# Kernel tuning notes

Measured on AMD Instinct MI355X. Metric: run time of the kernel, lower is better.

Reference implementation:

```python
import jax, jax.numpy as jnp
import numpy as np

B, N, D, H, NCB, TOPK = 4, 2048, 256, 2048, 256, 16
DP = D // 4
SCALE = float(np.sqrt(DP))
THRESH = 0.7
EPS = 1e-8


def setup_inputs() -> dict:
    key = jax.random.key(0)
    ks = jax.random.split(key, 12)
    g = lambda i, shape, s=1.0: jax.random.normal(ks[i], shape, jnp.float32) * s
    return {
        "agent_states": g(0, (B, N, D)),
        "agent_actions": g(1, (B, N, D)),
        "episodic_mem": g(2, (B, N, H)),
        "Wq": g(3, (D, DP), 0.05), "bq": jnp.zeros((DP,), jnp.float32),
        "Wk": g(4, (D, DP), 0.05), "bk": jnp.zeros((DP,), jnp.float32),
        "log_temp": jnp.asarray(0.0, jnp.float32),
        "Wc": g(5, (D, DP), 0.05), "bc": jnp.zeros((DP,), jnp.float32),
        "temp_coal": jnp.asarray(10.0, jnp.float32),
        "W_to_hdc": g(6, (D, H), 0.05), "b_to_hdc": jnp.zeros((H,), jnp.float32),
        "W_from_hdc": g(7, (H, D), 0.02), "b_from_hdc": jnp.zeros((D,), jnp.float32),
        "agent_keys": jnp.sign(g(8, (N, H))),
        "position_codes": jnp.sign(g(9, (NCB, H))),
        "step": 3,
    }


def _cosine(a, b):
    # torch F.cosine_similarity semantics, dim=-1, eps=1e-8
    na = jnp.maximum(jnp.linalg.norm(a, axis=-1), EPS)
    nb = jnp.maximum(jnp.linalg.norm(b, axis=-1), EPS)
    return jnp.sum(a * b, axis=-1) / (na * nb)


def _to_hdc_ste(x):
    soft = jnp.tanh(x * 3.0)
    hard = jnp.sign(x)
    hard = jnp.where(hard == 0, jnp.ones_like(hard), hard)
    return soft + jax.lax.stop_gradient(hard - soft)


def reference(agent_states, agent_actions, episodic_mem, Wq, bq, Wk, bk,
              log_temp, Wc, bc, temp_coal, W_to_hdc, b_to_hdc,
              W_from_hdc, b_from_hdc, agent_keys, position_codes, step):
    # ---- DynamicGraph.compute_graph: top-k dynamic attention adjacency ----
    Q = agent_actions @ Wq + bq                      # (B,N,DP)
    K = agent_actions @ Wk + bk                      # (B,N,DP)
    temp = jnp.clip(jnp.exp(log_temp), 0.1, 10.0)
    scores = jnp.einsum('bnd,bmd->bnm', Q, K) / (SCALE * temp)   # (B,N,N)
    _, topk_idx = jax.lax.top_k(scores, TOPK)                     # (B,N,k)
    bI = jnp.arange(B)[:, None, None]
    nI = jnp.arange(N)[None, :, None]
    mask = jnp.zeros_like(scores).at[bI, nI, topk_idx].set(1.0)   # scatter, like torch scatter_
    scores = scores * mask + (1.0 - mask) * -1e9
    adjacency = jax.nn.softmax(scores, axis=-1)
    # message passing over dynamic graph
    incoming = jnp.einsum('bnm,bmd->bnd', adjacency, agent_states)

    # ---- AgentCombination: sigmoid-normalized coalition mixing ----
    proj = agent_actions @ Wc + bc                   # (B,N,DP)
    pn = proj / jnp.maximum(jnp.linalg.norm(proj, axis=-1, keepdims=True), 1e-12)
    sim = jnp.einsum('bnd,bmd->bnm', pn, pn)
    cw = jax.nn.sigmoid((sim - THRESH) * temp_coal)
    cw = cw / (jnp.sum(cw, axis=-1, keepdims=True) + EPS)
    combined = jnp.einsum('bnm,bmd->bnd', cw, incoming)
    mixed = 0.8 * incoming + 0.2 * combined          # (B,N,D)

    # ---- HDCMemory: bind / write / read with STE ----
    q = _to_hdc_ste(mixed @ W_to_hdc + b_to_hdc)     # (B,N,H) bipolar via STE
    pq = q * agent_keys[None]                        # bind with agent key
    mem = jax.lax.stop_gradient(episodic_mem)        # memory read is detached in original
    pos_code = position_codes[step % NCB]            # (H,)
    new_mem = 0.95 * mem + 0.05 * (q * pos_code)     # write: bind + decay bundle
    strength = jax.nn.sigmoid(_cosine(new_mem, pq))[..., None]   # read similarity
    recall = (new_mem @ W_from_hdc + b_from_hdc) * strength      # (B,N,D)
    return mixed + recall
```

## Files before the change

### kernel.cpp

```cpp
#include <hip/hip_runtime.h>
#include <math.h>

#define BATCH 4
#define NN 2048
#define DD 256
#define HH 2048
#define DP 64
#define KTOP 16

typedef float f32x4 __attribute__((ext_vector_type(4)));
typedef short short8 __attribute__((ext_vector_type(8)));
typedef short short4v __attribute__((ext_vector_type(4)));

__device__ __forceinline__ short f2bf(float x) {
    union { float f; unsigned u; } v; v.f = x;
    unsigned r = v.u + 0x7FFFu + ((v.u >> 16) & 1u);
    return (short)(r >> 16);
}
__device__ __forceinline__ float bf2f(short s) {
    union { unsigned u; float f; } v; v.u = ((unsigned)(unsigned short)s) << 16;
    return v.f;
}

__global__ __launch_bounds__(64) void proj_kernel(
    const float* __restrict__ act,
    const float* __restrict__ Wq, const float* __restrict__ bq,
    const float* __restrict__ Wk, const float* __restrict__ bk,
    const float* __restrict__ Wc, const float* __restrict__ bc,
    float* __restrict__ Qo, float* __restrict__ Ko, short* __restrict__ Pno)
{
    const int row0 = blockIdx.x * 4;
    const int t = threadIdx.x;
    __shared__ float rowbuf[4][DD];
    const float* src = act + (size_t)row0 * DD;
    for (int i = t; i < 4 * DD; i += 64) rowbuf[i >> 8][i & 255] = src[i];
    __syncthreads();

    float q[4], k[4], c[4];
    #pragma unroll
    for (int r = 0; r < 4; ++r) { q[r] = bq[t]; k[r] = bk[t]; c[r] = bc[t]; }

    for (int d = 0; d < DD; ++d) {
        float wq = Wq[d * DP + t];
        float wk = Wk[d * DP + t];
        float wc = Wc[d * DP + t];
        #pragma unroll
        for (int r = 0; r < 4; ++r) {
            float av = rowbuf[r][d];
            q[r] = fmaf(av, wq, q[r]);
            k[r] = fmaf(av, wk, k[r]);
            c[r] = fmaf(av, wc, c[r]);
        }
    }
    #pragma unroll
    for (int r = 0; r < 4; ++r) {
        float ss = c[r] * c[r];
        #pragma unroll
        for (int off = 32; off; off >>= 1) ss += __shfl_xor(ss, off);
        float nrm = fmaxf(sqrtf(ss), 1e-12f);
        size_t o = (size_t)(row0 + r) * DP + t;
        Qo[o] = q[r];
        Ko[o] = k[r];
        Pno[o] = f2bf(c[r] / nrm);
    }
}

__global__ __launch_bounds__(256) void prep_kernel(
    const float* __restrict__ W2h, const float* __restrict__ Wfh,
    short* __restrict__ W2hT_hi, short* __restrict__ W2hT_lo,
    short* __restrict__ WfhT_hi, short* __restrict__ WfhT_lo)
{
    int b = blockIdx.x;
    const float* src; short *dhi, *dlo; int R, C, r0, c0;
    if (b < 512) {
        src = W2h; dhi = W2hT_hi; dlo = W2hT_lo; R = 256; C = 2048;
        r0 = (b >> 6) * 32; c0 = (b & 63) * 32;
    } else {
        b -= 512;
        src = Wfh; dhi = WfhT_hi; dlo = WfhT_lo; R = 2048; C = 256;
        r0 = (b >> 3) * 32; c0 = (b & 7) * 32;
    }
    int tx = threadIdx.x & 31, ty = threadIdx.x >> 5;
    __shared__ float tile[32][33];
    #pragma unroll
    for (int i = 0; i < 4; ++i)
        tile[ty + 8 * i][tx] = src[(size_t)(r0 + ty + 8 * i) * C + c0 + tx];
    __syncthreads();
    #pragma unroll
    for (int i = 0; i < 4; ++i) {
        float v = tile[tx][ty + 8 * i];
        short hi = f2bf(v);
        size_t o = (size_t)(c0 + ty + 8 * i) * R + r0 + tx;
        dhi[o] = hi;
        dlo[o] = f2bf(v - bf2f(hi));
    }
}

__global__ __launch_bounds__(512, 4) void attn_score_kernel(
    const float* __restrict__ Q, const float* __restrict__ K,
    const float* __restrict__ log_temp,
    float* __restrict__ selw_g, int* __restrict__ seli_g)
{
    const int t = threadIdx.x;
    const int w = t >> 6, l = t & 63;
    const int row = blockIdx.x * 8 + w;
    const int b = row >> 11;

    __shared__ float Ksh[128][68];

    const float temp = fminf(fmaxf(expf(log_temp[0]), 0.1f), 10.0f);
    const float scale = 1.0f / (8.0f * temp);

    const float* Kb = K + (size_t)b * NN * DP;
    const float4* qr4 = (const float4*)(Q + (size_t)row * DP);

    float sc[32];

    for (int ch = 0; ch < 16; ++ch) {
        __syncthreads();
        {
            int r = t >> 2, seg = t & 3;
            const float4* src = (const float4*)(Kb + (size_t)(ch * 128 + r) * DP + seg * 16);
            float4* dst = (float4*)&Ksh[r][seg * 16];
            dst[0] = src[0]; dst[1] = src[1]; dst[2] = src[2]; dst[3] = src[3];
        }
        __syncthreads();
        float a0 = 0.f, a1 = 0.f;
        const float4* k0 = (const float4*)&Ksh[l][0];
        const float4* k1 = (const float4*)&Ksh[64 + l][0];
        #pragma unroll
        for (int h = 0; h < 2; ++h) {
            float4 q[8];
            #pragma unroll
            for (int i = 0; i < 8; ++i) q[i] = qr4[h * 8 + i];
            #pragma unroll
            for (int i = 0; i < 8; ++i) {
                float4 kv0 = k0[h * 8 + i];
                float4 kv1 = k1[h * 8 + i];
                a0 = fmaf(kv0.x, q[i].x, fmaf(kv0.y, q[i].y, fmaf(kv0.z, q[i].z, fmaf(kv0.w, q[i].w, a0))));
                a1 = fmaf(kv1.x, q[i].x, fmaf(kv1.y, q[i].y, fmaf(kv1.z, q[i].z, fmaf(kv1.w, q[i].w, a1))));
            }
        }
        sc[ch * 2]     = a0 * scale;
        sc[ch * 2 + 1] = a1 * scale;
    }

    float wv = 0.f; int wm = 0;
    for (int it = 0; it < KTOP; ++it) {
        float bv = sc[0]; int bs = 0;
        #pragma unroll
        for (int i = 1; i < 32; ++i) {
            bool g = sc[i] > bv;
            bv = g ? sc[i] : bv;
            bs = g ? i : bs;
        }
        int bm = (bs >> 1) * 128 + (bs & 1) * 64 + l;
        #pragma unroll
        for (int off = 1; off < 64; off <<= 1) {
            float ov = __shfl_xor(bv, off);
            int   om = __shfl_xor(bm, off);
            bool take = (ov > bv) || (ov == bv && om < bm);
            bv = take ? ov : bv;
            bm = take ? om : bm;
        }
        if (l == it) { wv = bv; wm = bm; }
        if ((bm & 63) == l) {
            int s = ((bm >> 7) << 1) | ((bm >> 6) & 1);
            #pragma unroll
            for (int i = 0; i < 32; ++i) if (s == i) sc[i] = -3.0e38f;
        }
    }

    float mx = __shfl(wv, 0);
    float e = (l < KTOP) ? expf(wv - mx) : 0.f;
    float Z = e;
    #pragma unroll
    for (int off = 1; off < 64; off <<= 1) Z += __shfl_xor(Z, off);
    if (l < KTOP) {
        selw_g[(size_t)row * KTOP + l] = e / Z;
        seli_g[(size_t)row * KTOP + l] = wm;
    }
}

__global__ __launch_bounds__(256) void gather_kernel(
    const float* __restrict__ selw_g, const int* __restrict__ seli_g,
    const float* __restrict__ states, float* __restrict__ incoming)
{
    const int t = threadIdx.x;
    const int w = t >> 6, l = t & 63;
    const int row = blockIdx.x * 4 + w;
    const int b = row >> 11;

    float wv = 0.f; int mi = 0;
    if (l < KTOP) {
        wv = selw_g[(size_t)row * KTOP + l];
        mi = seli_g[(size_t)row * KTOP + l];
    }
    const float* Sb = states + (size_t)b * NN * DD;
    f32x4 acc = (f32x4){0.f, 0.f, 0.f, 0.f};
    #pragma unroll
    for (int kk = 0; kk < KTOP; ++kk) {
        float wk = __shfl(wv, kk);
        int   ik = __shfl(mi, kk);
        const float4 v = *(const float4*)(Sb + (size_t)ik * DD + l * 4);
        acc[0] = fmaf(wk, v.x, acc[0]);
        acc[1] = fmaf(wk, v.y, acc[1]);
        acc[2] = fmaf(wk, v.z, acc[2]);
        acc[3] = fmaf(wk, v.w, acc[3]);
    }
    *(float4*)(incoming + (size_t)row * DD + l * 4) = *(float4*)&acc;
}

__global__ __launch_bounds__(256) void coal_kernel(
    const short* __restrict__ pnb_g, const float* __restrict__ incoming,
    const float* __restrict__ temp_coal, float* __restrict__ mixed)
{
    const int b  = blockIdx.x >> 7;
    const int rem = blockIdx.x & 127;
    const int n0 = (rem >> 1) * 32;
    const int dh = rem & 1;
    const int t = threadIdx.x;
    const int w = t >> 6;
    const int l = t & 63;

    __shared__ alignas(16) short pnA[32][72];
    __shared__ alignas(16) short pnB[64][72];
    __shared__ alignas(16) short cwt[32][72];
    __shared__ alignas(16) short incT[128][72];
    __shared__ float rowsum[32];

    const size_t bbase = (size_t)b * NN;

    {
        int r = t >> 3, k8 = (t & 7) * 8;
        *(short8*)&pnA[r][k8] = *(const short8*)(pnb_g + (bbase + n0 + r) * DP + k8);
    }
    if (t < 32) rowsum[t] = 0.0f;

    const float tc = temp_coal[0];

    f32x4 acc[2][2];
    #pragma unroll
    for (int i = 0; i < 2; ++i)
        #pragma unroll
        for (int j = 0; j < 2; ++j)
            acc[i][j] = (f32x4){0.f, 0.f, 0.f, 0.f};

    const int lrow = l & 15;
    const int lk   = (l >> 4) * 8;

    for (int ch = 0; ch < 32; ++ch) {
        const int m0 = ch * 64;
        __syncthreads();

        {
            int r = t >> 2, kq = (t & 3) * 16;
            const short* src = pnb_g + (bbase + m0 + r) * DP + kq;
            *(short8*)&pnB[r][kq]     = *(const short8*)src;
            *(short8*)&pnB[r][kq + 8] = *(const short8*)(src + 8);
        }
        {
            int d4 = t & 31;
            int mg = t >> 5;
            const float* incb = incoming + (bbase + m0) * DD + dh * 128 + d4 * 4;
            #pragma unroll
            for (int i = 0; i < 8; ++i) {
                int m = mg * 8 + i;
                float4 v = *(const float4*)(incb + (size_t)m * DD);
                int db = d4 * 4;
                incT[db + 0][m] = f2bf(v.x);
                incT[db + 1][m] = f2bf(v.y);
                incT[db + 2][m] = f2bf(v.z);
                incT[db + 3][m] = f2bf(v.w);
            }
        }
        __syncthreads();

        f32x4 sacc[2];
        sacc[0] = (f32x4){0.f, 0.f, 0.f, 0.f};
        sacc[1] = (f32x4){0.f, 0.f, 0.f, 0.f};
        #pragma unroll
        for (int ks = 0; ks < 2; ++ks) {
            short8 bfr = *(const short8*)&pnB[w * 16 + lrow][lk + ks * 32];
            short8 a0  = *(const short8*)&pnA[lrow][lk + ks * 32];
            short8 a1  = *(const short8*)&pnA[16 + lrow][lk + ks * 32];
            sacc[0] = __builtin_amdgcn_mfma_f32_16x16x32_bf16(a0, bfr, sacc[0], 0, 0, 0);
            sacc[1] = __builtin_amdgcn_mfma_f32_16x16x32_bf16(a1, bfr, sacc[1], 0, 0, 0);
        }
        #pragma unroll
        for (int rt = 0; rt < 2; ++rt) {
            #pragma unroll
            for (int j = 0; j < 4; ++j) {
                int rr = rt * 16 + (l >> 4) * 4 + j;
                int cc = w * 16 + lrow;
                float cv = 1.0f / (1.0f + expf(-(sacc[rt][j] - 0.7f) * tc));
                cwt[rr][cc] = f2bf(cv);
            }
        }
        __syncthreads();

        {
            int r = t >> 3, c8 = (t & 7) * 8;
            short8 cv = *(const short8*)&cwt[r][c8];
            float p = 0.f;
            #pragma unroll
            for (int j = 0; j < 8; ++j) p += bf2f(cv[j]);
            p += __shfl_xor(p, 1);
            p += __shfl_xor(p, 2);
            p += __shfl_xor(p, 4);
            if ((t & 7) == 0) rowsum[r] += p;
        }

        #pragma unroll
        for (int ks = 0; ks < 2; ++ks) {
            short8 a0 = *(const short8*)&cwt[lrow][lk + ks * 32];
            short8 a1 = *(const short8*)&cwt[16 + lrow][lk + ks * 32];
            #pragma unroll
            for (int ct = 0; ct < 2; ++ct) {
                short8 bfr = *(const short8*)&incT[w * 32 + ct * 16 + lrow][lk + ks * 32];
                acc[0][ct] = __builtin_amdgcn_mfma_f32_16x16x32_bf16(a0, bfr, acc[0][ct], 0, 0, 0);
                acc[1][ct] = __builtin_amdgcn_mfma_f32_16x16x32_bf16(a1, bfr, acc[1][ct], 0, 0, 0);
            }
        }
    }
    __syncthreads();

    #pragma unroll
    for (int rt = 0; rt < 2; ++rt) {
        #pragma unroll
        for (int ct = 0; ct < 2; ++ct) {
            #pragma unroll
            for (int j = 0; j < 4; ++j) {
                int rr = rt * 16 + (l >> 4) * 4 + j;
                int cc = w * 32 + ct * 16 + lrow;
                float inv = 1.0f / (rowsum[rr] + 1e-8f);
                float comb = acc[rt][ct][j] * inv;
                size_t gi = (bbase + n0 + rr) * DD + dh * 128 + cc;
                mixed[gi] = 0.8f * incoming[gi] + 0.2f * comb;
            }
        }
    }
}

__global__ __launch_bounds__(256) void hdcA_kernel(
    const float* __restrict__ mixed,
    const short* __restrict__ W2hT_hi, const short* __restrict__ W2hT_lo,
    const float* __restrict__ b2h,
    unsigned short* __restrict__ qbits)
{
    const int rb = blockIdx.x >> 3;
    const int hs = blockIdx.x & 7;
    const int row0 = rb * 32;
    const int hbase = hs * 256;
    const int t = threadIdx.x;
    const int w = t >> 6, l = t & 63;
    const int lr = l & 15, lg = l >> 4;

    __shared__ short Ahi[32][264], Alo[32][264];
    __shared__ short Whi[64][136], Wlo[64][136];

    #pragma unroll
    for (int i = 0; i < 8; ++i) {
        int idx = t + i * 256;
        int r = idx >> 6, c = (idx & 63) * 4;
        float4 v = *(const float4*)(mixed + (size_t)(row0 + r) * DD + c);
        short4v hi4, lo4;
        hi4[0] = f2bf(v.x); lo4[0] = f2bf(v.x - bf2f(hi4[0]));
        hi4[1] = f2bf(v.y); lo4[1] = f2bf(v.y - bf2f(hi4[1]));
        hi4[2] = f2bf(v.z); lo4[2] = f2bf(v.z - bf2f(hi4[2]));
        hi4[3] = f2bf(v.w); lo4[3] = f2bf(v.w - bf2f(hi4[3]));
        *(short4v*)&Ahi[r][c] = hi4;
        *(short4v*)&Alo[r][c] = lo4;
    }

    for (int ch = 0; ch < 4; ++ch) {
        const int h0 = hbase + ch * 64;
        f32x4 zac[2];
        zac[0] = (f32x4){0.f, 0.f, 0.f, 0.f};
        zac[1] = (f32x4){0.f, 0.f, 0.f, 0.f};
        #pragma unroll
        for (int ks = 0; ks < 2; ++ks) {
            const int k0 = ks * 128;
            __syncthreads();
            {
                int r = t >> 2, cb = (t & 3) * 32;
                const short* sh = W2hT_hi + (size_t)(h0 + r) * DD + k0 + cb;
                const short* sl = W2hT_lo + (size_t)(h0 + r) * DD + k0 + cb;
                #pragma unroll
                for (int j = 0; j < 4; ++j) {
                    *(short8*)&Whi[r][cb + j * 8] = *(const short8*)(sh + j * 8);
                    *(short8*)&Wlo[r][cb + j * 8] = *(const short8*)(sl + j * 8);
                }
            }
            __syncthreads();
            #pragma unroll
            for (int kt = 0; kt < 4; ++kt) {
                int kk = k0 + kt * 32 + lg * 8;
                int kw = kt * 32 + lg * 8;
                short8 bhi = *(const short8*)&Whi[w * 16 + lr][kw];
                short8 blo = *(const short8*)&Wlo[w * 16 + lr][kw];
                #pragma unroll
                for (int mt = 0; mt < 2; ++mt) {
                    short8 ahi = *(const short8*)&Ahi[mt * 16 + lr][kk];
                    short8 alo = *(const short8*)&Alo[mt * 16 + lr][kk];
                    zac[mt] = __builtin_amdgcn_mfma_f32_16x16x32_bf16(ahi, bhi, zac[mt], 0, 0, 0);
                    zac[mt] = __builtin_amdgcn_mfma_f32_16x16x32_bf16(ahi, blo, zac[mt], 0, 0, 0);
                    zac[mt] = __builtin_amdgcn_mfma_f32_16x16x32_bf16(alo, bhi, zac[mt], 0, 0, 0);
                }
            }
        }
        const float bv = b2h[h0 + w * 16 + lr];
        #pragma unroll
        for (int mt = 0; mt < 2; ++mt) {
            #pragma unroll
            for (int j = 0; j < 4; ++j) {
                float z = zac[mt][j] + bv;
                unsigned long long bal = __ballot(z >= 0.0f);
                if (lr == 0)
                    qbits[(size_t)(row0 + mt * 16 + lg * 4 + j) * 128 + (h0 >> 4) + w] =
                        (unsigned short)((bal >> (lg * 16)) & 0xFFFFull);
            }
        }
    }
}

__global__ __launch_bounds__(512) void hdcB_kernel(
    const float* __restrict__ mem, const unsigned short* __restrict__ qbits,
    const float* __restrict__ pos_codes, const int* __restrict__ step,
    const short* __restrict__ WfhT_hi,
    const float* __restrict__ bfh, const float* __restrict__ keys,
    const float* __restrict__ mixed, float* __restrict__ out)
{
    const int mb = blockIdx.x >> 1, nb = blockIdx.x & 1;
    const int row0 = mb * 64, d0 = nb * 128;
    const int t = threadIdx.x;
    const int w = t >> 6, l = t & 63;
    const int wm = w >> 1, wn = w & 1;
    const int lr = l & 15, lg = l >> 4;

    __shared__ short Ahi[64][72], Alo[64][72];
    __shared__ short Bhi[128][72];
    __shared__ float sred[64][2];
    __shared__ float strenL[64];

    int st = ((step[0] % 256) + 256) % 256;
    const float* pos = pos_codes + (size_t)st * HH;

    f32x4 acc[4];
    #pragma unroll
    for (int i = 0; i < 4; ++i) acc[i] = (f32x4){0.f, 0.f, 0.f, 0.f};
    float pnum = 0.f, pns = 0.f;

    const int ar = t >> 3;
    const int ah = (t & 7) * 8;
    const int arow = row0 + ar;
    const size_t memb = (size_t)arow * HH;
    const size_t keyb = (size_t)(arow & (NN - 1)) * HH;

    for (int kc = 0; kc < 32; ++kc) {
        const int h0 = kc * 64;
        __syncthreads();
        {
            float mv[8], kv[8], pv[8];
            *(float4*)&mv[0] = *(const float4*)(mem + memb + h0 + ah);
            *(float4*)&mv[4] = *(const float4*)(mem + memb + h0 + ah + 4);
            *(float4*)&kv[0] = *(const float4*)(keys + keyb + h0 + ah);
            *(float4*)&kv[4] = *(const float4*)(keys + keyb + h0 + ah + 4);
            *(float4*)&pv[0] = *(const float4*)(pos + h0 + ah);
            *(float4*)&pv[4] = *(const float4*)(pos + h0 + ah + 4);
            unsigned bits = (unsigned)qbits[(size_t)arow * 128 + ((h0 + ah) >> 4)] >> (ah & 8);
            short hi8[8], lo8[8];
            #pragma unroll
            for (int j = 0; j < 8; ++j) {
                float q = ((bits >> j) & 1u) ? 1.0f : -1.0f;
                float nmv = fmaf(0.05f * q, pv[j], 0.95f * mv[j]);
                pnum = fmaf(nmv, q * kv[j], pnum);
                pns  = fmaf(nmv, nmv, pns);
                hi8[j] = f2bf(nmv);
                lo8[j] = f2bf(nmv - bf2f(hi8[j]));
            }
            *(short8*)&Ahi[ar][ah] = *(short8*)hi8;
            *(short8*)&Alo[ar][ah] = *(short8*)lo8;
        }
        {
            int r = t >> 2, hb = (t & 3) * 16;
            const short* sh = WfhT_hi + (size_t)(d0 + r) * HH + h0 + hb;
            *(short8*)&Bhi[r][hb]     = *(const short8*)sh;
            *(short8*)&Bhi[r][hb + 8] = *(const short8*)(sh + 8);
        }
        __syncthreads();
        #pragma unroll
        for (int kt = 0; kt < 2; ++kt) {
            const int kk = kt * 32 + lg * 8;
            short8 ahi = *(const short8*)&Ahi[wm * 16 + lr][kk];
            short8 alo = *(const short8*)&Alo[wm * 16 + lr][kk];
            #pragma unroll
            for (int nt = 0; nt < 4; ++nt) {
                short8 bhi = *(const short8*)&Bhi[wn * 64 + nt * 16 + lr][kk];
                acc[nt] = __builtin_amdgcn_mfma_f32_16x16x32_bf16(ahi, bhi, acc[nt], 0, 0, 0);
                acc[nt] = __builtin_amdgcn_mfma_f32_16x16x32_bf16(alo, bhi, acc[nt], 0, 0, 0);
            }
        }
    }

    #pragma unroll
    for (int off = 1; off < 8; off <<= 1) {
        pnum += __shfl_xor(pnum, off);
        pns  += __shfl_xor(pns, off);
    }
    if ((t & 7) == 0) { sred[ar][0] = pnum; sred[ar][1] = pns; }
    __syncthreads();
    if (t < 64) {
        float cosv = sred[t][0] / (fmaxf(sqrtf(sred[t][1]), 1e-8f) * sqrtf(2048.0f));
        strenL[t] = 1.0f / (1.0f + expf(-cosv));
    }
    __syncthreads();

    #pragma unroll
    for (int nt = 0; nt < 4; ++nt) {
        #pragma unroll
        for (int j = 0; j < 4; ++j) {
            int rloc = wm * 16 + lg * 4 + j;
            int col = d0 + wn * 64 + nt * 16 + lr;
            size_t gi = (size_t)(row0 + rloc) * DD + col;
            out[gi] = mixed[gi] + (acc[nt][j] + bfh[col]) * strenL[rloc];
        }
    }
}

extern "C" void kernel_launch(void* const* d_in, const int* in_sizes, int n_in,
                              void* d_out, int out_size, void* d_ws, size_t ws_size,
                              hipStream_t stream) {
    const float* states    = (const float*)d_in[0];
    const float* actions   = (const float*)d_in[1];
    const float* mem       = (const float*)d_in[2];
    const float* Wq        = (const float*)d_in[3];
    const float* bq        = (const float*)d_in[4];
    const float* Wk        = (const float*)d_in[5];
    const float* bk        = (const float*)d_in[6];
    const float* log_temp  = (const float*)d_in[7];
    const float* Wc        = (const float*)d_in[8];
    const float* bc        = (const float*)d_in[9];
    const float* temp_coal = (const float*)d_in[10];
    const float* W2h       = (const float*)d_in[11];
    const float* b2h       = (const float*)d_in[12];
    const float* Wfh       = (const float*)d_in[13];
    const float* bfh       = (const float*)d_in[14];
    const float* keys      = (const float*)d_in[15];
    const float* pos_codes = (const float*)d_in[16];
    const int*   step      = (const int*)d_in[17];
    float* out = (float*)d_out;

    float* ws = (float*)d_ws;
    float* mixed    = ws;
    short* W2hT_hi  = (short*)(mixed + 2097152);
    short* W2hT_lo  = W2hT_hi + 524288;
    short* WfhT_hi  = W2hT_lo + 524288;
    short* WfhT_lo  = WfhT_hi + 524288;
    unsigned short* qbits = (unsigned short*)(WfhT_lo + 524288);
    float* Q        = (float*)(qbits + 1048576);
    float* K        = Q + 524288;
    float* incoming = K + 524288;
    short* pn_bf    = (short*)(incoming + 2097152);
    float* selw     = (float*)(pn_bf + 524288);
    int*   seli     = (int*)(selw + 131072);

    proj_kernel<<<BATCH * NN / 4, 64, 0, stream>>>(actions, Wq, bq, Wk, bk, Wc, bc, Q, K, pn_bf);
    prep_kernel<<<1024, 256, 0, stream>>>(W2h, Wfh, W2hT_hi, W2hT_lo, WfhT_hi, WfhT_lo);
    attn_score_kernel<<<BATCH * NN / 8, 512, 0, stream>>>(Q, K, log_temp, selw, seli);
    gather_kernel<<<BATCH * NN / 4, 256, 0, stream>>>(selw, seli, states, incoming);
    coal_kernel<<<BATCH * (NN / 32) * 2, 256, 0, stream>>>(pn_bf, incoming, temp_coal, mixed);
    hdcA_kernel<<<(BATCH * NN / 32) * 8, 256, 0, stream>>>(mixed, W2hT_hi, W2hT_lo, b2h, qbits);
    hdcB_kernel<<<(BATCH * NN / 64) * 2, 512, 0, stream>>>(mem, qbits, pos_codes, step,
                                                           WfhT_hi, bfh, keys, mixed, out);
}
```

Before: 364.3 us.

## Split attention top-k across two half-waves and shrink HDC read tile rows

The attention score kernel now runs 1024 threads per block. Two groups of waves each score half of the key columns for the same 8 rows into a swizzled shared K tile, and each group keeps its own top-16. The two partial lists are merged through shared memory using packed 64-bit value/index keys. Separately, the hdcB kernel tile drops from 64 to 32 rows with four column waves, doubling its grid to improve parallelism and occupancy. The cost is more redundant loading of the B operand (WfhT) and the extra merge pass.

Measured after the change: 398.7 us. +9.4%, slower.

```diff
diff --git a/kernel.cpp b/kernel.cpp
--- a/kernel.cpp
+++ b/kernel.cpp
@@ -20,6 +20,11 @@
 __device__ __forceinline__ float bf2f(short s) {
     union { unsigned u; float f; } v; v.u = ((unsigned)(unsigned short)s) << 16;
     return v.f;
+}
+__device__ __forceinline__ unsigned long long shfl_xor_u64(unsigned long long v, int off) {
+    unsigned lo = (unsigned)v, hi = (unsigned)(v >> 32);
+    lo = __shfl_xor(lo, off); hi = __shfl_xor(hi, off);
+    return ((unsigned long long)hi << 32) | lo;
 }
 
 __global__ __launch_bounds__(64) void proj_kernel(
@@ -96,17 +101,20 @@
     }
 }
 
-__global__ __launch_bounds__(512, 4) void attn_score_kernel(
+#define KSWZ(r, c4) ((c4) ^ ((r) & 15))
+__global__ __launch_bounds__(1024) void attn_score_kernel(
     const float* __restrict__ Q, const float* __restrict__ K,
     const float* __restrict__ log_temp,
     float* __restrict__ selw_g, int* __restrict__ seli_g)
 {
     const int t = threadIdx.x;
     const int w = t >> 6, l = t & 63;
-    const int row = blockIdx.x * 8 + w;
+    const int half = w >> 3, rowLocal = w & 7;
+    const int row = blockIdx.x * 8 + rowLocal;
     const int b = row >> 11;
 
-    __shared__ float Ksh[128][68];
+    __shared__ float Ksh[2][128][64];
+    __shared__ unsigned long long mergeBuf[8][32];
 
     const float temp = fminf(fmaxf(expf(log_temp[0]), 0.1f), 10.0f);
     const float scale = 1.0f / (8.0f * temp);
@@ -114,47 +122,46 @@
     const float* Kb = K + (size_t)b * NN * DP;
     const float4* qr4 = (const float4*)(Q + (size_t)row * DP);
 
-    float sc[32];
-
-    for (int ch = 0; ch < 16; ++ch) {
+    float sc[16];
+
+    const int sr  = t >> 3;
+    const int sc4 = (t & 7) * 2;
+
+    for (int i = 0; i < 8; ++i) {
         __syncthreads();
-        {
-            int r = t >> 2, seg = t & 3;
-            const float4* src = (const float4*)(Kb + (size_t)(ch * 128 + r) * DP + seg * 16);
-            float4* dst = (float4*)&Ksh[r][seg * 16];
-            dst[0] = src[0]; dst[1] = src[1]; dst[2] = src[2]; dst[3] = src[3];
+        #pragma unroll
+        for (int p = 0; p < 2; ++p) {
+            const float4* src = (const float4*)(Kb + (size_t)(p * 1024 + i * 128 + sr) * DP) + sc4;
+            float4 v0 = src[0], v1 = src[1];
+            *(float4*)&Ksh[p][sr][KSWZ(sr, sc4) * 4]     = v0;
+            *(float4*)&Ksh[p][sr][KSWZ(sr, sc4 + 1) * 4] = v1;
         }
         __syncthreads();
-        float a0 = 0.f, a1 = 0.f;
-        const float4* k0 = (const float4*)&Ksh[l][0];
-        const float4* k1 = (const float4*)&Ksh[64 + l][0];
-        #pragma unroll
-        for (int h = 0; h < 2; ++h) {
-            float4 q[8];
-            #pragma unroll
-            for (int i = 0; i < 8; ++i) q[i] = qr4[h * 8 + i];
-            #pragma unroll
-            for (int i = 0; i < 8; ++i) {
-                float4 kv0 = k0[h * 8 + i];
-                float4 kv1 = k1[h * 8 + i];
-                a0 = fmaf(kv0.x, q[i].x, fmaf(kv0.y, q[i].y, fmaf(kv0.z, q[i].z, fmaf(kv0.w, q[i].w, a0))));
-                a1 = fmaf(kv1.x, q[i].x, fmaf(kv1.y, q[i].y, fmaf(kv1.z, q[i].z, fmaf(kv1.w, q[i].w, a1))));
-            }
-        }
-        sc[ch * 2]     = a0 * scale;
-        sc[ch * 2 + 1] = a1 * scale;
+        #pragma unroll
+        for (int sub = 0; sub < 2; ++sub) {
+            const int krow = sub * 64 + l;
+            const float* kr = &Ksh[half][krow][0];
+            float a = 0.f;
+            #pragma unroll
+            for (int c4 = 0; c4 < 16; ++c4) {
+                float4 kv = *(const float4*)&kr[KSWZ(krow, c4) * 4];
+                float4 qv = qr4[c4];
+                a = fmaf(kv.x, qv.x, fmaf(kv.y, qv.y, fmaf(kv.z, qv.z, fmaf(kv.w, qv.w, a))));
+            }
+            sc[i * 2 + sub] = a * scale;
+        }
     }
 
     float wv = 0.f; int wm = 0;
     for (int it = 0; it < KTOP; ++it) {
         float bv = sc[0]; int bs = 0;
         #pragma unroll
-        for (int i = 1; i < 32; ++i) {
+        for (int i = 1; i < 16; ++i) {
             bool g = sc[i] > bv;
             bv = g ? sc[i] : bv;
             bs = g ? i : bs;
         }
-        int bm = (bs >> 1) * 128 + (bs & 1) * 64 + l;
+        int bm = half * 1024 + (bs >> 1) * 128 + (bs & 1) * 64 + l;
         #pragma unroll
         for (int off = 1; off < 64; off <<= 1) {
             float ov = __shfl_xor(bv, off);
@@ -165,20 +172,46 @@
         }
         if (l == it) { wv = bv; wm = bm; }
         if ((bm & 63) == l) {
-            int s = ((bm >> 7) << 1) | ((bm >> 6) & 1);
-            #pragma unroll
-            for (int i = 0; i < 32; ++i) if (s == i) sc[i] = -3.0e38f;
-        }
-    }
-
-    float mx = __shfl(wv, 0);
-    float e = (l < KTOP) ? expf(wv - mx) : 0.f;
-    float Z = e;
-    #pragma unroll
-    for (int off = 1; off < 64; off <<= 1) Z += __shfl_xor(Z, off);
-    if (l < KTOP) {
-        selw_g[(size_t)row * KTOP + l] = e / Z;
-        seli_g[(size_t)row * KTOP + l] = wm;
+            int s = ((bm >> 7) & 7) * 2 + ((bm >> 6) & 1);
+            #pragma unroll
+            for (int i = 0; i < 16; ++i) if (s == i) sc[i] = -3.0e38f;
+        }
+    }
+
+    {
+        unsigned vb = __float_as_uint(wv);
+        unsigned vu = vb ^ (unsigned)(((int)vb >> 31) | 0x80000000);
+        unsigned long long key = ((unsigned long long)vu << 32) | (unsigned)(~wm);
+        if (l < KTOP) mergeBuf[rowLocal][half * 16 + l] = key;
+    }
+    __syncthreads();
+    if (half == 0) {
+        unsigned long long cand = (l < 32) ? mergeBuf[rowLocal][l] : 0ull;
+        float mwv = 0.f; int mwm = 0;
+        for (int it = 0; it < KTOP; ++it) {
+            unsigned long long best = cand;
+            #pragma unroll
+            for (int off = 1; off < 64; off <<= 1) {
+                unsigned long long o = shfl_xor_u64(best, off);
+                best = o > best ? o : best;
+            }
+            if (cand == best) cand = 0;
+            if (l == it) {
+                unsigned u = (unsigned)(best >> 32);
+                unsigned bb = (u & 0x80000000u) ? (u ^ 0x80000000u) : ~u;
+                mwv = __uint_as_float(bb);
+                mwm = (int)((~(unsigned)best) & (NN - 1));
+            }
+        }
+        float mx = __shfl(mwv, 0);
+        float e = (l < KTOP) ? expf(mwv - mx) : 0.f;
+        float Z = e;
+        #pragma unroll
+        for (int off = 1; off < 64; off <<= 1) Z += __shfl_xor(Z, off);
+        if (l < KTOP) {
+            selw_g[(size_t)row * KTOP + l] = e / Z;
+            seli_g[(size_t)row * KTOP + l] = mwm;
+        }
     }
 }
 
@@ -432,27 +465,27 @@
     const float* __restrict__ mixed, float* __restrict__ out)
 {
     const int mb = blockIdx.x >> 1, nb = blockIdx.x & 1;
-    const int row0 = mb * 64, d0 = nb * 128;
+    const int row0 = mb * 32, d0 = nb * 128;
     const int t = threadIdx.x;
     const int w = t >> 6, l = t & 63;
-    const int wm = w >> 1, wn = w & 1;
+    const int wm = w >> 2, wn = w & 3;
     const int lr = l & 15, lg = l >> 4;
 
-    __shared__ short Ahi[64][72], Alo[64][72];
+    __shared__ short Ahi[32][72], Alo[32][72];
     __shared__ short Bhi[128][72];
-    __shared__ float sred[64][2];
-    __shared__ float strenL[64];
+    __shared__ float sred[32][2];
+    __shared__ float strenL[32];
 
     int st = ((step[0] % 256) + 256) % 256;
     const float* pos = pos_codes + (size_t)st * HH;
 
-    f32x4 acc[4];
-    #pragma unroll
-    for (int i = 0; i < 4; ++i) acc[i] = (f32x4){0.f, 0.f, 0.f, 0.f};
+    f32x4 acc[2];
+    acc[0] = (f32x4){0.f, 0.f, 0.f, 0.f};
+    acc[1] = (f32x4){0.f, 0.f, 0.f, 0.f};
     float pnum = 0.f, pns = 0.f;
 
-    const int ar = t >> 3;
-    const int ah = (t & 7) * 8;
+    const int ar = t >> 4;
+    const int ah = (t & 15) * 4;
     const int arow = row0 + ar;
     const size_t memb = (size_t)arow * HH;
     const size_t keyb = (size_t)(arow & (NN - 1)) * HH;
@@ -461,26 +494,25 @@
         const int h0 = kc * 64;
         __syncthreads();
         {
-            float mv[8], kv[8], pv[8];
-            *(float4*)&mv[0] = *(const float4*)(mem + memb + h0 + ah);
-            *(float4*)&mv[4] = *(const float4*)(mem + memb + h0 + ah + 4);
-            *(float4*)&kv[0] = *(const float4*)(keys + keyb + h0 + ah);
-            *(float4*)&kv[4] = *(const float4*)(keys + keyb + h0 + ah + 4);
-            *(float4*)&pv[0] = *(const float4*)(pos + h0 + ah);
-            *(float4*)&pv[4] = *(const float4*)(pos + h0 + ah + 4);
-            unsigned bits = (unsigned)qbits[(size_t)arow * 128 + ((h0 + ah) >> 4)] >> (ah & 8);
-            short hi8[8], lo8[8];
-            #pragma unroll
-            for (int j = 0; j < 8; ++j) {
+            float4 mv = *(const float4*)(mem + memb + h0 + ah);
+            float4 kv = *(const float4*)(keys + keyb + h0 + ah);
+            float4 pv = *(const float4*)(pos + h0 + ah);
+            unsigned bits = (unsigned)qbits[(size_t)arow * 128 + ((h0 + ah) >> 4)] >> (ah & 15);
+            float mvs[4] = { mv.x, mv.y, mv.z, mv.w };
+            float kvs[4] = { kv.x, kv.y, kv.z, kv.w };
+            float pvs[4] = { pv.x, pv.y, pv.z, pv.w };
+            short4v hi4, lo4;
+            #pragma unroll
+            for (int j = 0; j < 4; ++j) {
                 float q = ((bits >> j) & 1u) ? 1.0f : -1.0f;
-                float nmv = fmaf(0.05f * q, pv[j], 0.95f * mv[j]);
-                pnum = fmaf(nmv, q * kv[j], pnum);
+                float nmv = fmaf(0.05f * q, pvs[j], 0.95f * mvs[j]);
+                pnum = fmaf(nmv, q * kvs[j], pnum);
                 pns  = fmaf(nmv, nmv, pns);
-                hi8[j] = f2bf(nmv);
-                lo8[j] = f2bf(nmv - bf2f(hi8[j]));
-            }
-            *(short8*)&Ahi[ar][ah] = *(short8*)hi8;
-            *(short8*)&Alo[ar][ah] = *(short8*)lo8;
+                hi4[j] = f2bf(nmv);
+                lo4[j] = f2bf(nmv - bf2f(hi4[j]));
+            }
+            *(short4v*)&Ahi[ar][ah] = hi4;
+            *(short4v*)&Alo[ar][ah] = lo4;
         }
         {
             int r = t >> 2, hb = (t & 3) * 16;
@@ -495,8 +527,8 @@
             short8 ahi = *(const short8*)&Ahi[wm * 16 + lr][kk];
             short8 alo = *(const short8*)&Alo[wm * 16 + lr][kk];
             #pragma unroll
-            for (int nt = 0; nt < 4; ++nt) {
-                short8 bhi = *(const short8*)&Bhi[wn * 64 + nt * 16 + lr][kk];
+            for (int nt = 0; nt < 2; ++nt) {
+                short8 bhi = *(const short8*)&Bhi[wn * 32 + nt * 16 + lr][kk];
                 acc[nt] = __builtin_amdgcn_mfma_f32_16x16x32_bf16(ahi, bhi, acc[nt], 0, 0, 0);
                 acc[nt] = __builtin_amdgcn_mfma_f32_16x16x32_bf16(alo, bhi, acc[nt], 0, 0, 0);
             }
@@ -504,24 +536,24 @@
     }
 
     #pragma unroll
-    for (int off = 1; off < 8; off <<= 1) {
+    for (int off = 1; off < 16; off <<= 1) {
         pnum += __shfl_xor(pnum, off);
         pns  += __shfl_xor(pns, off);
     }
-    if ((t & 7) == 0) { sred[ar][0] = pnum; sred[ar][1] = pns; }
+    if ((t & 15) == 0) { sred[ar][0] = pnum; sred[ar][1] = pns; }
     __syncthreads();
-    if (t < 64) {
+    if (t < 32) {
         float cosv = sred[t][0] / (fmaxf(sqrtf(sred[t][1]), 1e-8f) * sqrtf(2048.0f));
         strenL[t] = 1.0f / (1.0f + expf(-cosv));
     }
     __syncthreads();
 
     #pragma unroll
-    for (int nt = 0; nt < 4; ++nt) {
+    for (int nt = 0; nt < 2; ++nt) {
         #pragma unroll
         for (int j = 0; j < 4; ++j) {
             int rloc = wm * 16 + lg * 4 + j;
-            int col = d0 + wn * 64 + nt * 16 + lr;
+            int col = d0 + wn * 32 + nt * 16 + lr;
             size_t gi = (size_t)(row0 + rloc) * DD + col;
             out[gi] = mixed[gi] + (acc[nt][j] + bfh[col]) * strenL[rloc];
         }
@@ -567,10 +599,10 @@
 
     proj_kernel<<<BATCH * NN / 4, 64, 0, stream>>>(actions, Wq, bq, Wk, bk, Wc, bc, Q, K, pn_bf);
     prep_kernel<<<1024, 256, 0, stream>>>(W2h, Wfh, W2hT_hi, W2hT_lo, WfhT_hi, WfhT_lo);
-    attn_score_kernel<<<BATCH * NN / 8, 512, 0, stream>>>(Q, K, log_temp, selw, seli);
+    attn_score_kernel<<<BATCH * NN / 8, 1024, 0, stream>>>(Q, K, log_temp, selw, seli);
     gather_kernel<<<BATCH * NN / 4, 256, 0, stream>>>(selw, seli, states, incoming);
     coal_kernel<<<BATCH * (NN / 32) * 2, 256, 0, stream>>>(pn_bf, incoming, temp_coal, mixed);
     hdcA_kernel<<<(BATCH * NN / 32) * 8, 256, 0, stream>>>(mixed, W2hT_hi, W2hT_lo, b2h, qbits);
-    hdcB_kernel<<<(BATCH * NN / 64) * 2, 512, 0, stream>>>(mem, qbits, pos_codes, step,
+    hdcB_kernel<<<(BATCH * NN / 32) * 2, 512, 0, stream>>>(mem, qbits, pos_codes, step,
                                                            WfhT_hi, bfh, keys, mixed, out);
 }
```
